# Performance work log

Measured on AMD Instinct MI355X. Metric: run time of the kernel, lower is better.

## Reference

```python
import jax, jax.numpy as jnp
import numpy as np

# Model dims (see init_kwargs / shape_source)
B = 2048      # batch
CIN = 256     # tabular input features (c_in)
NH = 512      # TabularEncoder hidden width
NENC_HID = 4  # nlayers=6 -> input layer + 4 hidden + output layer
NF = 112      # n_features = num_concepts (conv=False path)
K = 112       # num_concepts
NL = 50       # num_latent_concepts
MC = 100      # num_monte_carlo
NOUT = 200    # num_output


def setup_inputs() -> dict:
    key = jax.random.key(0)
    ks = jax.random.split(key, 8)
    x = jax.random.normal(ks[0], (B, CIN), dtype=jnp.float32)
    enc_Win = jax.random.normal(ks[1], (CIN, NH), dtype=jnp.float32) * (1.0 / np.sqrt(CIN))
    enc_bin = jnp.zeros((NH,), jnp.float32)
    enc_Wh = jax.random.normal(ks[2], (NENC_HID, NH, NH), dtype=jnp.float32) * (1.0 / np.sqrt(NH))
    enc_bh = jnp.zeros((NENC_HID, NH), jnp.float32)
    enc_Wout = jax.random.normal(ks[3], (NH, NF), dtype=jnp.float32) * (1.0 / np.sqrt(NH))
    enc_bout = jnp.zeros((NF,), jnp.float32)
    # Per-concept predictor i has first Linear of shape [NF+i, NL]; pad all to [NF+K, NL]
    # and statically slice rows [:NF+i] in the loop (unused padded rows never touched).
    pred_W1 = jax.random.normal(ks[4], (K, NF + K, NL), dtype=jnp.float32) * (1.0 / np.sqrt(NF))
    pred_b1 = jnp.zeros((K, NL), jnp.float32)
    pred_W2 = jax.random.normal(ks[5], (K, NL), dtype=jnp.float32) * (1.0 / np.sqrt(NL))
    pred_b2 = jnp.zeros((K,), jnp.float32)
    head_W = jax.random.normal(ks[6], (K, NOUT), dtype=jnp.float32) * (1.0 / np.sqrt(K))
    head_b = jnp.zeros((NOUT,), jnp.float32)
    return {
        "x": x,
        "enc_Win": enc_Win, "enc_bin": enc_bin,
        "enc_Wh": enc_Wh, "enc_bh": enc_bh,
        "enc_Wout": enc_Wout, "enc_bout": enc_bout,
        "pred_W1": pred_W1, "pred_b1": pred_b1,
        "pred_W2": pred_W2, "pred_b2": pred_b2,
        "head_W": head_W, "head_b": head_b,
        "epoch": 0,
    }


def reference(x, enc_Win, enc_bin, enc_Wh, enc_bh, enc_Wout, enc_bout,
              pred_W1, pred_b1, pred_W2, pred_b2, head_W, head_b, epoch):
    lrelu = jax.nn.leaky_relu  # negative_slope=0.01, matches nn.LeakyReLU default

    # ---- TabularEncoder (ni=CIN, nhidden=NH, nlayers=6, no=NF) ----
    h = lrelu(x @ enc_Win + enc_bin)
    for i in range(enc_Wh.shape[0]):
        h = lrelu(h @ enc_Wh[i] + enc_bh[i])
    inter = h @ enc_Wout + enc_bout                      # [B, NF]
    Bn = inter.shape[0]

    key = jax.random.key(42)
    c_hard = jnp.zeros((Bn, K, MC), inter.dtype)
    c_probs = []
    for i in range(K):
        W1 = pred_W1[i, :NF + i]                          # [NF+i, NL]
        base = inter @ W1[:NF] + pred_b1[i]               # [B, NL], shared across MC
        if i == 0:
            p1 = jax.nn.sigmoid(lrelu(base) @ pred_W2[i] + pred_b2[i])   # [B]
            p = jnp.broadcast_to(p1[:, None], (Bn, MC))   # expand(-1,-1,MC)
        else:
            # add contribution of the i previously sampled hard concepts, per MC sample
            hpre = base[:, None, :] + jnp.einsum('bim,ih->bmh', c_hard[:, :i], W1[NF:])  # [B,MC,NL]
            p = jax.nn.sigmoid(jnp.einsum('bmh,h->bm', lrelu(hpre), pred_W2[i]) + pred_b2[i])  # [B,MC]
        key, sk = jax.random.split(key)
        samp = jax.random.bernoulli(sk, p).astype(p.dtype)  # torch.bernoulli(concept)
        c_hard = c_hard.at[:, i, :].set(samp)
        c_probs.append(p)

    c_prob = jnp.stack(c_probs, axis=1)                   # [B, K, MC]

    # ---- Head: MC average of softmax probabilities (pred_dim > 1 branch) ----
    logits = jnp.einsum('bkm,ko->bmo', c_hard, head_W) + head_b   # [B, MC, NOUT]
    probs = jax.nn.softmax(logits, axis=-1).mean(axis=1)          # [B, NOUT]
    y_pred_logits = jnp.log(probs + 1e-6)
    return (c_prob, y_pred_logits, c_hard)
```

## Files before the change

### kernel.cpp

```cpp
#include <hip/hip_runtime.h>

typedef unsigned int u32;
typedef unsigned short u16;
typedef unsigned long long u64;

#define YOFF  22937600ull
#define CHOFF 23347200ull

#define OFF_HA    0ull
#define OFF_HB    4194304ull
#define OFF_INTER 8388608ull

__host__ __device__ inline u32 rotl32_(u32 x, int r) { return (x << r) | (x >> (32 - r)); }
__host__ __device__ inline void tf2x32(u32 k0, u32 k1, u32 c0, u32 c1, u32& o0, u32& o1) {
  u32 ks0 = k0, ks1 = k1, ks2 = k0 ^ k1 ^ 0x1BD11BDAu;
  u32 x0 = c0 + ks0, x1 = c1 + ks1;
  const int RA[4] = {13, 15, 26, 6}, RB[4] = {17, 29, 16, 24};
  for (int i = 0; i < 5; ++i) {
    const int* R = (i & 1) ? RB : RA;
    for (int j = 0; j < 4; ++j) { x0 += x1; x1 = rotl32_(x1, R[j]); x1 ^= x0; }
    switch (i) {
      case 0: x0 += ks1; x1 += ks2 + 1u; break;
      case 1: x0 += ks2; x1 += ks0 + 2u; break;
      case 2: x0 += ks0; x1 += ks1 + 3u; break;
      case 3: x0 += ks1; x1 += ks2 + 4u; break;
      case 4: x0 += ks2; x1 += ks0 + 5u; break;
    }
  }
  o0 = x0; o1 = x1;
}

struct SKeys { u32 v[224]; };

template <bool DO_LRELU>
__global__ __launch_bounds__(256) void gemm_bias(const float* __restrict__ A,
                                                 const float* __restrict__ Bm,
                                                 const float* __restrict__ bias,
                                                 float* __restrict__ C,
                                                 int M, int N, int K) {
  __shared__ float As[32][65];
  __shared__ float Bs[32][65];
  const int bm = blockIdx.y * 64, bn = blockIdx.x * 64;
  const int t = threadIdx.x;
  const int ty = t >> 4, tx = t & 15;
  float acc[4][4] = {};
  for (int k0 = 0; k0 < K; k0 += 32) {
#pragma unroll
    for (int l = 0; l < 2; ++l) {
      int e = l * 256 + t;
      int m = e >> 3, k4 = e & 7;
      float4 v = *(const float4*)(A + (size_t)(bm + m) * K + (k0 + k4 * 4));
      As[k4 * 4 + 0][m] = v.x; As[k4 * 4 + 1][m] = v.y;
      As[k4 * 4 + 2][m] = v.z; As[k4 * 4 + 3][m] = v.w;
    }
#pragma unroll
    for (int l = 0; l < 2; ++l) {
      int e = l * 256 + t;
      int k = e >> 4, n4 = e & 15;
      int gn = bn + n4 * 4;
      if (gn < N) {
        float4 v = *(const float4*)(Bm + (size_t)(k0 + k) * N + gn);
        Bs[k][n4 * 4 + 0] = v.x; Bs[k][n4 * 4 + 1] = v.y;
        Bs[k][n4 * 4 + 2] = v.z; Bs[k][n4 * 4 + 3] = v.w;
      } else {
        Bs[k][n4 * 4 + 0] = 0.f; Bs[k][n4 * 4 + 1] = 0.f;
        Bs[k][n4 * 4 + 2] = 0.f; Bs[k][n4 * 4 + 3] = 0.f;
      }
    }
    __syncthreads();
#pragma unroll
    for (int kk = 0; kk < 32; ++kk) {
      float a[4], b[4];
#pragma unroll
      for (int j = 0; j < 4; ++j) { a[j] = As[kk][ty * 4 + j]; b[j] = Bs[kk][tx * 4 + j]; }
#pragma unroll
      for (int i = 0; i < 4; ++i)
#pragma unroll
        for (int j = 0; j < 4; ++j) acc[i][j] = fmaf(a[i], b[j], acc[i][j]);
    }
    __syncthreads();
  }
#pragma unroll
  for (int i = 0; i < 4; ++i) {
#pragma unroll
    for (int j = 0; j < 4; ++j) {
      int m = bm + ty * 4 + i, n = bn + tx * 4 + j;
      if (n < N) {
        float s = acc[i][j] + bias[n];
        if (DO_LRELU) { if (s < 0.f) s = 0.01f * s; }
        C[(size_t)m * N + n] = s;
      }
    }
  }
}

__global__ __launch_bounds__(256) void base_kernel(const float* __restrict__ inter,
                                                   const float* __restrict__ W1,
                                                   const float* __restrict__ pb1,
                                                   float* __restrict__ out) {
  __shared__ float As[112][65];
  __shared__ float Ws[112][64];
  const int i = blockIdx.y;
  const int b0 = blockIdx.x * 64;
  const int t = threadIdx.x;
  const int ty = t >> 4, tx = t & 15;
#pragma unroll
  for (int l = 0; l < 7; ++l) {
    int e4 = l * 256 + t;
    int k4 = e4 % 28, bs = e4 / 28;
    float4 v = *(const float4*)(inter + (size_t)(b0 + bs) * 112 + k4 * 4);
    As[k4 * 4 + 0][bs] = v.x; As[k4 * 4 + 1][bs] = v.y;
    As[k4 * 4 + 2][bs] = v.z; As[k4 * 4 + 3][bs] = v.w;
  }
#pragma unroll
  for (int l = 0; l < 28; ++l) {
    int e = l * 256 + t;
    int r = e >> 6, c = e & 63;
    Ws[r][c] = (c < 50) ? W1[(size_t)i * 11200 + r * 50 + c] : 0.f;
  }
  __syncthreads();
  float acc[4][4] = {};
  for (int kk = 0; kk < 112; ++kk) {
    float a[4], b[4];
#pragma unroll
    for (int j = 0; j < 4; ++j) { a[j] = As[kk][ty * 4 + j]; b[j] = Ws[kk][tx * 4 + j]; }
#pragma unroll
    for (int ii = 0; ii < 4; ++ii)
#pragma unroll
      for (int j = 0; j < 4; ++j) acc[ii][j] = fmaf(a[ii], b[j], acc[ii][j]);
  }
#pragma unroll
  for (int ii = 0; ii < 4; ++ii) {
#pragma unroll
    for (int j = 0; j < 4; ++j) {
      int b = b0 + ty * 4 + ii, h = tx * 4 + j;
      if (h < 50) {
        out[CHOFF + (size_t)b * 11200 + (size_t)i * 100 + h] = acc[ii][j] + pb1[i * 50 + h];
      }
    }
  }
}

__global__ __launch_bounds__(512) void sample_kernel(const float* __restrict__ W1,
                                                     const float* __restrict__ W2,
                                                     const float* __restrict__ b2,
                                                     float* __restrict__ out, SKeys sks) {
  const int t = threadIdx.x;
  const int p = blockIdx.x * 500 + t;
  const bool active = (t < 500) && (p < 204800);
  const int b = p / 100;
  const int m = p - b * 100;
  const size_t rowbase = (size_t)b * 11200 + m;
  const float* __restrict__ baserow = out + CHOFF + (size_t)b * 11200;
  u64 lo = 0, hi = 0;

  if (active) {
    for (int i = 0; i < 112; ++i) {
      const float* __restrict__ Wi = W1 + (size_t)i * 11200 + 5600;
      float acc[50];
#pragma unroll
      for (int h = 0; h < 50; ++h) acc[h] = 0.f;
      for (int r = 0; r < i; ++r) {
        float c = (((r < 64) ? (lo >> r) : (hi >> (r - 64))) & 1ull) ? 1.f : 0.f;
        const float* __restrict__ wr = Wi + r * 50;
#pragma unroll
        for (int h = 0; h < 50; ++h) acc[h] = fmaf(c, wr[h], acc[h]);
      }
      const float* __restrict__ w2 = W2 + i * 50;
      const float* bs = baserow + (size_t)i * 100;
      float s = 0.f;
#pragma unroll
      for (int h = 0; h < 50; ++h) {
        float v = acc[h] + bs[h];
        if (v < 0.f) v = 0.01f * v;
        s = fmaf(v, w2[h], s);
      }
      float l = s + b2[i];
      float pr = 1.f / (1.f + expf(-l));
      u32 a0, a1;
      tf2x32(sks.v[2 * i], sks.v[2 * i + 1], 0u, (u32)p, a0, a1);
      u32 fb = ((a0 ^ a1) >> 9) | 0x3F800000u;
      float u; __builtin_memcpy(&u, &fb, 4); u -= 1.f;
      int smp = (u < pr) ? 1 : 0;
      out[rowbase + (size_t)i * 100] = pr;
      if (smp) { if (i < 64) lo |= 1ull << i; else hi |= 1ull << (i - 64); }
    }
    for (int i = 0; i < 112; ++i) {
      u64 bit = (i < 64) ? (lo >> i) : (hi >> (i - 64));
      out[CHOFF + rowbase + (size_t)i * 100] = (bit & 1ull) ? 1.0f : 0.0f;
    }
  }
}

__global__ __launch_bounds__(256) void head_kernel(const float* __restrict__ HW,
                                                   const float* __restrict__ hb,
                                                   float* __restrict__ out) {
  __shared__ unsigned char cS[100][116];
  __shared__ float lgS[50][201];
  const int b = blockIdx.x;
  const int t = threadIdx.x;
  for (int e = t; e < 11200; e += 256) {
    int k = e / 100, m = e - k * 100;
    cS[m][k] = (out[CHOFF + (size_t)b * 11200 + (size_t)k * 100 + m] != 0.f) ? 1 : 0;
  }
  __syncthreads();
  float pacc = 0.f;
  for (int mh = 0; mh < 2; ++mh) {
    for (int l = 0; l < 3; ++l) {
      int tile = l * 256 + t;
      if (tile < 625) {
        int o0 = (tile % 25) * 8;
        int m0 = (tile / 25) * 2;
        float acc[2][8] = {};
        for (int k = 0; k < 112; ++k) {
          float4 wa = *(const float4*)(HW + (size_t)k * 200 + o0);
          float4 wb = *(const float4*)(HW + (size_t)k * 200 + o0 + 4);
          float w[8] = {wa.x, wa.y, wa.z, wa.w, wb.x, wb.y, wb.z, wb.w};
          float c0 = (float)cS[mh * 50 + m0][k];
          float c1 = (float)cS[mh * 50 + m0 + 1][k];
#pragma unroll
          for (int jo = 0; jo < 8; ++jo) {
            acc[0][jo] = fmaf(c0, w[jo], acc[0][jo]);
            acc[1][jo] = fmaf(c1, w[jo], acc[1][jo]);
          }
        }
#pragma unroll
        for (int im = 0; im < 2; ++im)
#pragma unroll
          for (int jo = 0; jo < 8; ++jo) {
            int o = o0 + jo;
            lgS[m0 + im][o] = acc[im][jo] + hb[o];
          }
      }
    }
    __syncthreads();
    if (t < 50) {
      int m = t;
      float mx = -3.0e38f;
      for (int o = 0; o < 200; ++o) mx = fmaxf(mx, lgS[m][o]);
      float s = 0.f;
      for (int o = 0; o < 200; ++o) {
        float e = expf(lgS[m][o] - mx);
        lgS[m][o] = e; s += e;
      }
      float inv = 1.f / s;
      for (int o = 0; o < 200; ++o) lgS[m][o] = lgS[m][o] * inv;
    }
    __syncthreads();
    if (t < 200) { for (int m = 0; m < 50; ++m) pacc += lgS[m][t]; }
    __syncthreads();
  }
  if (t < 200) {
    out[YOFF + (size_t)b * 200 + t] = logf(pacc / 100.f + 1e-6f);
  }
}

extern "C" void kernel_launch(void* const* d_in, const int* in_sizes, int n_in,
                              void* d_out, int out_size, void* d_ws, size_t ws_size,
                              hipStream_t stream) {
  const float* x    = (const float*)d_in[0];
  const float* Win  = (const float*)d_in[1];
  const float* bin  = (const float*)d_in[2];
  const float* Wh   = (const float*)d_in[3];
  const float* bh   = (const float*)d_in[4];
  const float* Wout = (const float*)d_in[5];
  const float* bout = (const float*)d_in[6];
  const float* pW1  = (const float*)d_in[7];
  const float* pb1  = (const float*)d_in[8];
  const float* pW2  = (const float*)d_in[9];
  const float* pb2  = (const float*)d_in[10];
  const float* hW   = (const float*)d_in[11];
  const float* hb   = (const float*)d_in[12];
  float* out = (float*)d_out;
  char* ws = (char*)d_ws;

  float* hA     = (float*)(ws + OFF_HA);
  float* hB     = (float*)(ws + OFF_HB);
  float* interB = (float*)(ws + OFF_INTER);

  gemm_bias<true ><<<dim3(8, 32), 256, 0, stream>>>(x,  Win,             bin,          hA,     2048, 512, 256);
  gemm_bias<true ><<<dim3(8, 32), 256, 0, stream>>>(hA, Wh + 0 * 262144, bh + 0 * 512, hB,     2048, 512, 512);
  gemm_bias<true ><<<dim3(8, 32), 256, 0, stream>>>(hB, Wh + 1 * 262144, bh + 1 * 512, hA,     2048, 512, 512);
  gemm_bias<true ><<<dim3(8, 32), 256, 0, stream>>>(hA, Wh + 2 * 262144, bh + 2 * 512, hB,     2048, 512, 512);
  gemm_bias<true ><<<dim3(8, 32), 256, 0, stream>>>(hB, Wh + 3 * 262144, bh + 3 * 512, hA,     2048, 512, 512);
  gemm_bias<false><<<dim3(2, 32), 256, 0, stream>>>(hA, Wout,            bout,         interB, 2048, 112, 512);

  base_kernel<<<dim3(32, 112), 256, 0, stream>>>(interB, pW1, pb1, out);

  SKeys sks;
  {
    u32 k0 = 0u, k1 = 42u;
    for (int i = 0; i < 112; ++i) {
      u32 nk0, nk1, s0, s1;
      tf2x32(k0, k1, 0u, 0u, nk0, nk1);
      tf2x32(k0, k1, 0u, 1u, s0, s1);
      sks.v[2 * i] = s0; sks.v[2 * i + 1] = s1;
      k0 = nk0; k1 = nk1;
    }
  }
  sample_kernel<<<410, 512, 0, stream>>>(pW1, pW2, pb2, out, sks);

  head_kernel<<<2048, 256, 0, stream>>>(hW, hb, out);
}
```

Before: 3.718 ms.

## Split sequential sampling hidden dim across two warps and defer hard-concept expansion

Each (batch, MC) sample's 50-wide hidden accumulation in the sequential concept loop is now split across two wavefronts, 25 each, and partial activations are exchanged through shared memory every concept step. The goal is to cut per-thread register pressure and raise occupancy on the latency-bound serial loop, using 1600 blocks of 256 threads instead of 410 of 512. Sampled bits are packed into 32-bit words in scratch space within the c_hard region and expanded to floats by a separate kernel. The cost is two block barriers per concept iteration and an extra kernel launch.

Result: slower. 9.650 ms (+159.5%).

```diff
diff --git a/kernel.cpp b/kernel.cpp
--- a/kernel.cpp
+++ b/kernel.cpp
@@ -141,54 +141,121 @@
   }
 }
 
-__global__ __launch_bounds__(512) void sample_kernel(const float* __restrict__ W1,
-                                                     const float* __restrict__ W2,
-                                                     const float* __restrict__ b2,
-                                                     float* __restrict__ out, SKeys sks) {
-  const int t = threadIdx.x;
-  const int p = blockIdx.x * 500 + t;
-  const bool active = (t < 500) && (p < 204800);
+__global__ __launch_bounds__(256, 7) void sample_kernel2(const float* __restrict__ W1,
+                                                         const float* __restrict__ W2,
+                                                         const float* __restrict__ b2,
+                                                         float* __restrict__ out, SKeys sks) {
+  __shared__ float vbuf[128][26];
+  __shared__ u32 bitbuf[128];
+  const int t = threadIdx.x;
+  const int w = t >> 6;
+  const int lane = t & 63;
+  const int sub = w >> 1;
+  const int q = ((w & 1) << 6) | lane;
+  const int p = blockIdx.x * 128 + q;
   const int b = p / 100;
   const int m = p - b * 100;
-  const size_t rowbase = (size_t)b * 11200 + m;
   const float* __restrict__ baserow = out + CHOFF + (size_t)b * 11200;
   u64 lo = 0, hi = 0;
 
-  if (active) {
-    for (int i = 0; i < 112; ++i) {
-      const float* __restrict__ Wi = W1 + (size_t)i * 11200 + 5600;
-      float acc[50];
-#pragma unroll
-      for (int h = 0; h < 50; ++h) acc[h] = 0.f;
-      for (int r = 0; r < i; ++r) {
-        float c = (((r < 64) ? (lo >> r) : (hi >> (r - 64))) & 1ull) ? 1.f : 0.f;
+  for (int i = 0; i < 112; ++i) {
+    const float* __restrict__ Wi = W1 + (size_t)i * 11200 + 5600 + sub * 25;
+    float acc[25];
+#pragma unroll
+    for (int h = 0; h < 25; ++h) acc[h] = 0.f;
+    {
+      int r = 0;
+      int r1 = (i < 64) ? i : 64;
+      u64 cm = lo;
+      for (; r < r1; ++r) {
+        float c = (cm & 1ull) ? 1.f : 0.f;
+        cm >>= 1;
         const float* __restrict__ wr = Wi + r * 50;
 #pragma unroll
-        for (int h = 0; h < 50; ++h) acc[h] = fmaf(c, wr[h], acc[h]);
-      }
-      const float* __restrict__ w2 = W2 + i * 50;
-      const float* bs = baserow + (size_t)i * 100;
-      float s = 0.f;
-#pragma unroll
-      for (int h = 0; h < 50; ++h) {
-        float v = acc[h] + bs[h];
-        if (v < 0.f) v = 0.01f * v;
-        s = fmaf(v, w2[h], s);
-      }
-      float l = s + b2[i];
-      float pr = 1.f / (1.f + expf(-l));
+        for (int h = 0; h < 25; ++h) acc[h] = fmaf(c, wr[h], acc[h]);
+      }
+      cm = hi;
+      for (; r < i; ++r) {
+        float c = (cm & 1ull) ? 1.f : 0.f;
+        cm >>= 1;
+        const float* __restrict__ wr = Wi + r * 50;
+#pragma unroll
+        for (int h = 0; h < 25; ++h) acc[h] = fmaf(c, wr[h], acc[h]);
+      }
+    }
+    const float* bs = baserow + (size_t)i * 100 + sub * 25;
+    if (sub) {
+#pragma unroll
+      for (int h2 = 0; h2 < 12; ++h2) {
+        float v0 = acc[2 * h2] + bs[2 * h2];         if (v0 < 0.f) v0 = 0.01f * v0;
+        float v1 = acc[2 * h2 + 1] + bs[2 * h2 + 1]; if (v1 < 0.f) v1 = 0.01f * v1;
+        *(float2*)&vbuf[q][2 * h2] = make_float2(v0, v1);
+      }
+      {
+        float v24 = acc[24] + bs[24]; if (v24 < 0.f) v24 = 0.01f * v24;
+        vbuf[q][24] = v24;
+      }
       u32 a0, a1;
       tf2x32(sks.v[2 * i], sks.v[2 * i + 1], 0u, (u32)p, a0, a1);
       u32 fb = ((a0 ^ a1) >> 9) | 0x3F800000u;
       float u; __builtin_memcpy(&u, &fb, 4); u -= 1.f;
-      int smp = (u < pr) ? 1 : 0;
-      out[rowbase + (size_t)i * 100] = pr;
-      if (smp) { if (i < 64) lo |= 1ull << i; else hi |= 1ull << (i - 64); }
-    }
-    for (int i = 0; i < 112; ++i) {
-      u64 bit = (i < 64) ? (lo >> i) : (hi >> (i - 64));
-      out[CHOFF + rowbase + (size_t)i * 100] = (bit & 1ull) ? 1.0f : 0.0f;
-    }
+      vbuf[q][25] = u;
+    }
+    __syncthreads();
+    if (!sub) {
+      const float* __restrict__ w2 = W2 + i * 50;
+      float s = 0.f;
+#pragma unroll
+      for (int h = 0; h < 25; ++h) {
+        float v = acc[h] + bs[h];
+        if (v < 0.f) v = 0.01f * v;
+        s = fmaf(v, w2[h], s);
+      }
+#pragma unroll
+      for (int h2 = 0; h2 < 12; ++h2) {
+        float2 vv = *(const float2*)&vbuf[q][2 * h2];
+        s = fmaf(vv.x, w2[25 + 2 * h2], s);
+        s = fmaf(vv.y, w2[26 + 2 * h2], s);
+      }
+      s = fmaf(vbuf[q][24], w2[49], s);
+      float l = s + b2[i];
+      float pr = 1.f / (1.f + expf(-l));
+      float u = vbuf[q][25];
+      u32 smp = (u < pr) ? 1u : 0u;
+      out[(size_t)b * 11200 + (size_t)i * 100 + m] = pr;
+      bitbuf[q] = smp;
+    }
+    __syncthreads();
+    u32 bit = bitbuf[q];
+    if (bit) { if (i < 64) lo |= 1ull << i; else hi |= 1ull << (i - 64); }
+  }
+  if (!sub) {
+    u32* ob = (u32*)out;
+    size_t cb = CHOFF + (size_t)b * 11200 + (size_t)((m >= 50) ? 4 : 0) * 100 + 50 + (m % 50);
+    ob[cb + 0]   = (u32)lo;
+    ob[cb + 100] = (u32)(lo >> 32);
+    ob[cb + 200] = (u32)hi;
+    ob[cb + 300] = (u32)(hi >> 32);
+  }
+}
+
+__global__ __launch_bounds__(256) void expand_kernel(float* __restrict__ out) {
+  __shared__ u32 mW[100][4];
+  const int b = blockIdx.x;
+  const int t = threadIdx.x;
+  const u32* ob = (const u32*)out;
+  if (t < 100) {
+    size_t cb = CHOFF + (size_t)b * 11200 + (size_t)((t >= 50) ? 4 : 0) * 100 + 50 + (t % 50);
+    mW[t][0] = ob[cb + 0];
+    mW[t][1] = ob[cb + 100];
+    mW[t][2] = ob[cb + 200];
+    mW[t][3] = ob[cb + 300];
+  }
+  __syncthreads();
+  for (int e = t; e < 11200; e += 256) {
+    int i = e / 100, m = e - i * 100;
+    u32 word = mW[m][i >> 5];
+    out[CHOFF + (size_t)b * 11200 + e] = (float)((word >> (i & 31)) & 1u);
   }
 }
 
@@ -298,7 +365,8 @@
       k0 = nk0; k1 = nk1;
     }
   }
-  sample_kernel<<<410, 512, 0, stream>>>(pW1, pW2, pb2, out, sks);
+  sample_kernel2<<<1600, 256, 0, stream>>>(pW1, pW2, pb2, out, sks);
+  expand_kernel<<<2048, 256, 0, stream>>>(out);
 
   head_kernel<<<2048, 256, 0, stream>>>(hW, hb, out);
 }
```

## Double-buffer sample accumulators to overlap next-step matvec with current sampling

Applied to the files above, without the earlier changes.

Restructures the sequential concept-sampling kernel so that the contribution of all previous hard concepts to step i+1 is accumulated while step i is being finalized. Only the newest sampled bit is applied afterwards, which shortens the dependent chain per step. The bitmask is packed into scratch slots and expanded to floats by a new kernel, instead of 112 strided float stores per thread. The launch moves to 256-thread blocks with an occupancy hint, at the cost of two 50-float accumulator arrays of register pressure and an extra kernel launch.

Measured after the change: 8.867 ms. +138.5%, slower.

```diff
diff --git a/kernel.cpp b/kernel.cpp
--- a/kernel.cpp
+++ b/kernel.cpp
@@ -141,54 +141,116 @@
   }
 }
 
-__global__ __launch_bounds__(512) void sample_kernel(const float* __restrict__ W1,
-                                                     const float* __restrict__ W2,
-                                                     const float* __restrict__ b2,
-                                                     float* __restrict__ out, SKeys sks) {
-  const int t = threadIdx.x;
-  const int p = blockIdx.x * 500 + t;
-  const bool active = (t < 500) && (p < 204800);
+__global__ __launch_bounds__(256, 3) void sample_kernel3(const float* __restrict__ W1,
+                                                         const float* __restrict__ W2,
+                                                         const float* __restrict__ b2v,
+                                                         float* __restrict__ out, SKeys sks) {
+  const int t = threadIdx.x;
+  const int p = blockIdx.x * 256 + t;
   const int b = p / 100;
   const int m = p - b * 100;
-  const size_t rowbase = (size_t)b * 11200 + m;
   const float* __restrict__ baserow = out + CHOFF + (size_t)b * 11200;
   u64 lo = 0, hi = 0;
-
-  if (active) {
-    for (int i = 0; i < 112; ++i) {
-      const float* __restrict__ Wi = W1 + (size_t)i * 11200 + 5600;
-      float acc[50];
-#pragma unroll
-      for (int h = 0; h < 50; ++h) acc[h] = 0.f;
-      for (int r = 0; r < i; ++r) {
-        float c = (((r < 64) ? (lo >> r) : (hi >> (r - 64))) & 1ull) ? 1.f : 0.f;
-        const float* __restrict__ wr = Wi + r * 50;
-#pragma unroll
-        for (int h = 0; h < 50; ++h) acc[h] = fmaf(c, wr[h], acc[h]);
-      }
-      const float* __restrict__ w2 = W2 + i * 50;
-      const float* bs = baserow + (size_t)i * 100;
-      float s = 0.f;
-#pragma unroll
-      for (int h = 0; h < 50; ++h) {
-        float v = acc[h] + bs[h];
-        if (v < 0.f) v = 0.01f * v;
-        s = fmaf(v, w2[h], s);
-      }
-      float l = s + b2[i];
-      float pr = 1.f / (1.f + expf(-l));
-      u32 a0, a1;
-      tf2x32(sks.v[2 * i], sks.v[2 * i + 1], 0u, (u32)p, a0, a1);
-      u32 fb = ((a0 ^ a1) >> 9) | 0x3F800000u;
-      float u; __builtin_memcpy(&u, &fb, 4); u -= 1.f;
-      int smp = (u < pr) ? 1 : 0;
-      out[rowbase + (size_t)i * 100] = pr;
-      if (smp) { if (i < 64) lo |= 1ull << i; else hi |= 1ull << (i - 64); }
-    }
-    for (int i = 0; i < 112; ++i) {
-      u64 bit = (i < 64) ? (lo >> i) : (hi >> (i - 64));
-      out[CHOFF + rowbase + (size_t)i * 100] = (bit & 1ull) ? 1.0f : 0.0f;
-    }
+  float accA[50], accB[50];
+#pragma unroll
+  for (int h = 0; h < 50; ++h) accA[h] = 0.f;
+
+#define STEP(I, ACC_C, ACC_N)                                                               \
+  {                                                                                         \
+    const int i = (I);                                                                      \
+      \
+    if (i < 111) {                                                                          \
+      const float* __restrict__ Wn = W1 + (size_t)(i + 1) * 11200 + 5600;                   \
+      _Pragma("unroll")                                                                     \
+      for (int h = 0; h < 50; ++h) ACC_N[h] = 0.f;                                          \
+      _Pragma("unroll")                                                                     \
+      for (int half = 0; half < 2; ++half) {                                                \
+        const float* __restrict__ Wh = Wn + half * 25;                                      \
+        int r = 0;                                                                          \
+        int r1 = (i < 64) ? i : 64;                                                         \
+        u64 cm = lo;                                                                        \
+        for (; r < r1; ++r) {                                                               \
+          float c = (cm & 1ull) ? 1.f : 0.f;                                                \
+          cm >>= 1;                                                                         \
+          const float* __restrict__ wr = Wh + r * 50;       \
+          _Pragma("unroll")                                                                 \
+          for (int h = 0; h < 25; ++h)                                                      \
+            ACC_N[half * 25 + h] = fmaf(c, wr[h], ACC_N[half * 25 + h]);                    \
+        }                                                                                   \
+        cm = hi;                                                                            \
+        for (; r < i; ++r) {                                                                \
+          float c = (cm & 1ull) ? 1.f : 0.f;                                                \
+          cm >>= 1;                                                                         \
+          const float* __restrict__ wr = Wh + r * 50;                                       \
+          _Pragma("unroll")                                                                 \
+          for (int h = 0; h < 25; ++h)                                                      \
+            ACC_N[half * 25 + h] = fmaf(c, wr[h], ACC_N[half * 25 + h]);                    \
+        }                                                                                   \
+      }                                                                                     \
+    }                                                                                       \
+          \
+    const float* __restrict__ w2 = W2 + i * 50;                           \
+    const float* bs = baserow + (size_t)i * 100;           \
+    float s = 0.f;                                                                          \
+    _Pragma("unroll")                                                                       \
+    for (int h = 0; h < 50; ++h) {                                                          \
+      float v = ACC_C[h] + bs[h];                                                           \
+      if (v < 0.f) v = 0.01f * v;                                                           \
+      s = fmaf(v, w2[h], s);                                                                \
+    }                                                                                       \
+    float l = s + b2v[i];                                                                   \
+    float pr = 1.f / (1.f + expf(-l));                                                      \
+    u32 a0, a1;                                                                             \
+    tf2x32(sks.v[2 * i], sks.v[2 * i + 1], 0u, (u32)p, a0, a1);                             \
+    u32 fb = ((a0 ^ a1) >> 9) | 0x3F800000u;                                                \
+    float uu; __builtin_memcpy(&uu, &fb, 4); uu -= 1.f;                                     \
+    float cbit = (uu < pr) ? 1.f : 0.f;                                                     \
+    out[(size_t)b * 11200 + (size_t)i * 100 + m] = pr;             \
+    {                                                                                       \
+      u64 sbit = (uu < pr) ? 1ull : 0ull;                                                   \
+      if (i < 64) lo |= sbit << i; else hi |= sbit << (i - 64);                             \
+    }                                                                                       \
+         \
+    if (i < 111) {                                                                          \
+      const float* __restrict__ wr = W1 + (size_t)(i + 1) * 11200 + 5600 + (size_t)i * 50;  \
+      _Pragma("unroll")                                                                     \
+      for (int h = 0; h < 50; ++h) ACC_N[h] = fmaf(cbit, wr[h], ACC_N[h]);                  \
+    }                                                                                       \
+  }
+
+  for (int i0 = 0; i0 < 112; i0 += 2) {
+    STEP(i0, accA, accB)
+    STEP(i0 + 1, accB, accA)
+  }
+#undef STEP
+
+  {
+    u32* ob = (u32*)out;
+    size_t cb = CHOFF + (size_t)b * 11200 + (size_t)((m >= 50) ? 4 : 0) * 100 + 50 + (m % 50);
+    ob[cb + 0]   = (u32)lo;
+    ob[cb + 100] = (u32)(lo >> 32);
+    ob[cb + 200] = (u32)hi;
+    ob[cb + 300] = (u32)(hi >> 32);
+  }
+}
+
+__global__ __launch_bounds__(256) void expand_kernel(float* __restrict__ out) {
+  __shared__ u32 mW[100][4];
+  const int b = blockIdx.x;
+  const int t = threadIdx.x;
+  const u32* ob = (const u32*)out;
+  if (t < 100) {
+    size_t cb = CHOFF + (size_t)b * 11200 + (size_t)((t >= 50) ? 4 : 0) * 100 + 50 + (t % 50);
+    mW[t][0] = ob[cb + 0];
+    mW[t][1] = ob[cb + 100];
+    mW[t][2] = ob[cb + 200];
+    mW[t][3] = ob[cb + 300];
+  }
+  __syncthreads();
+  for (int e = t; e < 11200; e += 256) {
+    int i = e / 100, m = e - i * 100;
+    u32 word = mW[m][i >> 5];
+    out[CHOFF + (size_t)b * 11200 + e] = (float)((word >> (i & 31)) & 1u);
   }
 }
 
@@ -298,7 +360,8 @@
       k0 = nk0; k1 = nk1;
     }
   }
-  sample_kernel<<<410, 512, 0, stream>>>(pW1, pW2, pb2, out, sks);
+  sample_kernel3<<<800, 256, 0, stream>>>(pW1, pW2, pb2, out, sks);
+  expand_kernel<<<2048, 256, 0, stream>>>(out);
 
   head_kernel<<<2048, 256, 0, stream>>>(hW, hb, out);
 }
```

## Split sample kernel hidden dim across thread pairs with repacked padded W1

Applied to the files above, without the earlier changes.

The sequential Bernoulli sampling kernel now assigns two threads per (batch, MC) sample, each handling 25 of the 50 hidden units and combining partial results through a lane shuffle. W1's concept rows are repacked into a padded 56-wide layout so weights load as float4. The base values are stored in a matching padded column layout. Sampled bits go to a compact mask buffer, and a separate expand kernel writes the float hard-concept output. The aim is more parallelism and occupancy (1600 blocks, fewer registers per thread) with vectorised loads, at the cost of an extra repack pass, an extra expand kernel and shuffle traffic.

Measured after the change: 9.523 ms. +156.1%, slower.

```diff
diff --git a/kernel.cpp b/kernel.cpp
--- a/kernel.cpp
+++ b/kernel.cpp
@@ -94,6 +94,16 @@
   }
 }
 
+__global__ __launch_bounds__(256) void repack_w1(const float* __restrict__ W1, float* __restrict__ Wp) {
+  const int i = blockIdx.x;
+  for (int e = threadIdx.x; e < 112 * 56; e += 256) {
+    int r = e / 56, c = e - r * 56;
+    int sub = c / 28, h = c - sub * 28;
+    float v = (h < 25) ? W1[(size_t)i * 11200 + 5600 + r * 50 + sub * 25 + h] : 0.f;
+    Wp[(size_t)i * 6272 + e] = v;
+  }
+}
+
 __global__ __launch_bounds__(256) void base_kernel(const float* __restrict__ inter,
                                                    const float* __restrict__ W1,
                                                    const float* __restrict__ pb1,
@@ -135,60 +145,140 @@
     for (int j = 0; j < 4; ++j) {
       int b = b0 + ty * 4 + ii, h = tx * 4 + j;
       if (h < 50) {
-        out[CHOFF + (size_t)b * 11200 + (size_t)i * 100 + h] = acc[ii][j] + pb1[i * 50 + h];
-      }
-    }
-  }
-}
-
-__global__ __launch_bounds__(512) void sample_kernel(const float* __restrict__ W1,
-                                                     const float* __restrict__ W2,
-                                                     const float* __restrict__ b2,
-                                                     float* __restrict__ out, SKeys sks) {
-  const int t = threadIdx.x;
-  const int p = blockIdx.x * 500 + t;
-  const bool active = (t < 500) && (p < 204800);
+        int col = (h < 25) ? h : h + 3;
+        out[CHOFF + (size_t)b * 11200 + (size_t)i * 100 + col] = acc[ii][j] + pb1[i * 50 + h];
+      }
+    }
+  }
+}
+
+__global__ __launch_bounds__(256, 5) void sample_kernel4(const float* __restrict__ Wp,
+                                                         const float* __restrict__ W2,
+                                                         const float* __restrict__ b2v,
+                                                         float* __restrict__ out,
+                                                         u32* __restrict__ masks, SKeys sks) {
+  const int t = threadIdx.x;
+  const int sub = t & 1;
+  const int p = blockIdx.x * 128 + (t >> 1);
   const int b = p / 100;
   const int m = p - b * 100;
-  const size_t rowbase = (size_t)b * 11200 + m;
-  const float* __restrict__ baserow = out + CHOFF + (size_t)b * 11200;
+  const float* __restrict__ baseb = out + CHOFF + (size_t)b * 11200 + sub * 28;
+  const float* __restrict__ Wsub = Wp + sub * 28;
   u64 lo = 0, hi = 0;
-
-  if (active) {
-    for (int i = 0; i < 112; ++i) {
-      const float* __restrict__ Wi = W1 + (size_t)i * 11200 + 5600;
-      float acc[50];
-#pragma unroll
-      for (int h = 0; h < 50; ++h) acc[h] = 0.f;
-      for (int r = 0; r < i; ++r) {
-        float c = (((r < 64) ? (lo >> r) : (hi >> (r - 64))) & 1ull) ? 1.f : 0.f;
-        const float* __restrict__ wr = Wi + r * 50;
-#pragma unroll
-        for (int h = 0; h < 50; ++h) acc[h] = fmaf(c, wr[h], acc[h]);
-      }
-      const float* __restrict__ w2 = W2 + i * 50;
-      const float* bs = baserow + (size_t)i * 100;
-      float s = 0.f;
-#pragma unroll
-      for (int h = 0; h < 50; ++h) {
-        float v = acc[h] + bs[h];
-        if (v < 0.f) v = 0.01f * v;
-        s = fmaf(v, w2[h], s);
-      }
-      float l = s + b2[i];
-      float pr = 1.f / (1.f + expf(-l));
-      u32 a0, a1;
-      tf2x32(sks.v[2 * i], sks.v[2 * i + 1], 0u, (u32)p, a0, a1);
-      u32 fb = ((a0 ^ a1) >> 9) | 0x3F800000u;
-      float u; __builtin_memcpy(&u, &fb, 4); u -= 1.f;
-      int smp = (u < pr) ? 1 : 0;
-      out[rowbase + (size_t)i * 100] = pr;
-      if (smp) { if (i < 64) lo |= 1ull << i; else hi |= 1ull << (i - 64); }
-    }
-    for (int i = 0; i < 112; ++i) {
-      u64 bit = (i < 64) ? (lo >> i) : (hi >> (i - 64));
-      out[CHOFF + rowbase + (size_t)i * 100] = (bit & 1ull) ? 1.0f : 0.0f;
-    }
+  float acc[25], rcv[25];
+
+  for (int i = 0; i < 112; ++i) {
+#pragma unroll
+    for (int h = 0; h < 25; ++h) acc[h] = 0.f;
+    {
+      const float* __restrict__ Wi = Wsub + (size_t)i * 6272;
+      int r = 0;
+      int r1 = (i < 64) ? i : 64;
+      u64 cm = lo;
+      for (; r < r1; ++r) {
+        float c = (cm & 1ull) ? 1.f : 0.f;
+        cm >>= 1;
+        const float* __restrict__ wr = Wi + r * 56;
+        float4 q0 = ((const float4*)wr)[0];
+        float4 q1 = ((const float4*)wr)[1];
+        float4 q2 = ((const float4*)wr)[2];
+        float4 q3 = ((const float4*)wr)[3];
+        float4 q4 = ((const float4*)wr)[4];
+        float4 q5 = ((const float4*)wr)[5];
+        float w24 = wr[24];
+        acc[0] = fmaf(c, q0.x, acc[0]);  acc[1] = fmaf(c, q0.y, acc[1]);
+        acc[2] = fmaf(c, q0.z, acc[2]);  acc[3] = fmaf(c, q0.w, acc[3]);
+        acc[4] = fmaf(c, q1.x, acc[4]);  acc[5] = fmaf(c, q1.y, acc[5]);
+        acc[6] = fmaf(c, q1.z, acc[6]);  acc[7] = fmaf(c, q1.w, acc[7]);
+        acc[8] = fmaf(c, q2.x, acc[8]);  acc[9] = fmaf(c, q2.y, acc[9]);
+        acc[10] = fmaf(c, q2.z, acc[10]); acc[11] = fmaf(c, q2.w, acc[11]);
+        acc[12] = fmaf(c, q3.x, acc[12]); acc[13] = fmaf(c, q3.y, acc[13]);
+        acc[14] = fmaf(c, q3.z, acc[14]); acc[15] = fmaf(c, q3.w, acc[15]);
+        acc[16] = fmaf(c, q4.x, acc[16]); acc[17] = fmaf(c, q4.y, acc[17]);
+        acc[18] = fmaf(c, q4.z, acc[18]); acc[19] = fmaf(c, q4.w, acc[19]);
+        acc[20] = fmaf(c, q5.x, acc[20]); acc[21] = fmaf(c, q5.y, acc[21]);
+        acc[22] = fmaf(c, q5.z, acc[22]); acc[23] = fmaf(c, q5.w, acc[23]);
+        acc[24] = fmaf(c, w24, acc[24]);
+      }
+      cm = hi;
+      for (; r < i; ++r) {
+        float c = (cm & 1ull) ? 1.f : 0.f;
+        cm >>= 1;
+        const float* __restrict__ wr = Wi + r * 56;
+        float4 q0 = ((const float4*)wr)[0];
+        float4 q1 = ((const float4*)wr)[1];
+        float4 q2 = ((const float4*)wr)[2];
+        float4 q3 = ((const float4*)wr)[3];
+        float4 q4 = ((const float4*)wr)[4];
+        float4 q5 = ((const float4*)wr)[5];
+        float w24 = wr[24];
+        acc[0] = fmaf(c, q0.x, acc[0]);  acc[1] = fmaf(c, q0.y, acc[1]);
+        acc[2] = fmaf(c, q0.z, acc[2]);  acc[3] = fmaf(c, q0.w, acc[3]);
+        acc[4] = fmaf(c, q1.x, acc[4]);  acc[5] = fmaf(c, q1.y, acc[5]);
+        acc[6] = fmaf(c, q1.z, acc[6]);  acc[7] = fmaf(c, q1.w, acc[7]);
+        acc[8] = fmaf(c, q2.x, acc[8]);  acc[9] = fmaf(c, q2.y, acc[9]);
+        acc[10] = fmaf(c, q2.z, acc[10]); acc[11] = fmaf(c, q2.w, acc[11]);
+        acc[12] = fmaf(c, q3.x, acc[12]); acc[13] = fmaf(c, q3.y, acc[13]);
+        acc[14] = fmaf(c, q3.z, acc[14]); acc[15] = fmaf(c, q3.w, acc[15]);
+        acc[16] = fmaf(c, q4.x, acc[16]); acc[17] = fmaf(c, q4.y, acc[17]);
+        acc[18] = fmaf(c, q4.z, acc[18]); acc[19] = fmaf(c, q4.w, acc[19]);
+        acc[20] = fmaf(c, q5.x, acc[20]); acc[21] = fmaf(c, q5.y, acc[21]);
+        acc[22] = fmaf(c, q5.z, acc[22]); acc[23] = fmaf(c, q5.w, acc[23]);
+        acc[24] = fmaf(c, w24, acc[24]);
+      }
+    }
+    {
+      const float* __restrict__ bs = baseb + (size_t)i * 100;
+#pragma unroll
+      for (int j = 0; j < 6; ++j) {
+        float4 q = ((const float4*)bs)[j];
+        float x;
+        x = acc[4 * j + 0] + q.x; acc[4 * j + 0] = (x < 0.f) ? 0.01f * x : x;
+        x = acc[4 * j + 1] + q.y; acc[4 * j + 1] = (x < 0.f) ? 0.01f * x : x;
+        x = acc[4 * j + 2] + q.z; acc[4 * j + 2] = (x < 0.f) ? 0.01f * x : x;
+        x = acc[4 * j + 3] + q.w; acc[4 * j + 3] = (x < 0.f) ? 0.01f * x : x;
+      }
+      float x = acc[24] + bs[24]; acc[24] = (x < 0.f) ? 0.01f * x : x;
+    }
+#pragma unroll
+    for (int h = 0; h < 25; ++h) rcv[h] = __shfl_xor(acc[h], 1, 64);
+    const float* __restrict__ w2 = W2 + i * 50;
+    float s = 0.f;
+#pragma unroll
+    for (int h = 0; h < 25; ++h) { float val = sub ? rcv[h] : acc[h]; s = fmaf(val, w2[h], s); }
+#pragma unroll
+    for (int h = 0; h < 25; ++h) { float val = sub ? acc[h] : rcv[h]; s = fmaf(val, w2[25 + h], s); }
+    float l = s + b2v[i];
+    float pr = 1.f / (1.f + expf(-l));
+    u32 a0, a1;
+    tf2x32(sks.v[2 * i], sks.v[2 * i + 1], 0u, (u32)p, a0, a1);
+    u32 fb = ((a0 ^ a1) >> 9) | 0x3F800000u;
+    float uu; __builtin_memcpy(&uu, &fb, 4); uu -= 1.f;
+    u64 sbit = (uu < pr) ? 1ull : 0ull;
+    if (!sub) out[(size_t)b * 11200 + (size_t)i * 100 + m] = pr;
+    if (i < 64) lo |= sbit << i; else hi |= sbit << (i - 64);
+  }
+  if (!sub) {
+    u32* mp = masks + (size_t)p * 4;
+    mp[0] = (u32)lo; mp[1] = (u32)(lo >> 32);
+    mp[2] = (u32)hi; mp[3] = (u32)(hi >> 32);
+  }
+}
+
+__global__ __launch_bounds__(256) void expand_kernel(const u32* __restrict__ masks,
+                                                     float* __restrict__ out) {
+  __shared__ u32 mW[100][4];
+  const int b = blockIdx.x;
+  const int t = threadIdx.x;
+  if (t < 100) {
+    const u32* mp = masks + ((size_t)b * 100 + t) * 4;
+    mW[t][0] = mp[0]; mW[t][1] = mp[1]; mW[t][2] = mp[2]; mW[t][3] = mp[3];
+  }
+  __syncthreads();
+  for (int e = t; e < 11200; e += 256) {
+    int i = e / 100, m = e - i * 100;
+    u32 word = mW[m][i >> 5];
+    out[CHOFF + (size_t)b * 11200 + e] = (float)((word >> (i & 31)) & 1u);
   }
 }
 
@@ -277,6 +367,8 @@
   float* hA     = (float*)(ws + OFF_HA);
   float* hB     = (float*)(ws + OFF_HB);
   float* interB = (float*)(ws + OFF_INTER);
+  float* Wp     = (float*)(ws + OFF_HA);
+  u32*   masks  = (u32*)(ws + OFF_HB);
 
   gemm_bias<true ><<<dim3(8, 32), 256, 0, stream>>>(x,  Win,             bin,          hA,     2048, 512, 256);
   gemm_bias<true ><<<dim3(8, 32), 256, 0, stream>>>(hA, Wh + 0 * 262144, bh + 0 * 512, hB,     2048, 512, 512);
@@ -284,6 +376,8 @@
   gemm_bias<true ><<<dim3(8, 32), 256, 0, stream>>>(hA, Wh + 2 * 262144, bh + 2 * 512, hB,     2048, 512, 512);
   gemm_bias<true ><<<dim3(8, 32), 256, 0, stream>>>(hB, Wh + 3 * 262144, bh + 3 * 512, hA,     2048, 512, 512);
   gemm_bias<false><<<dim3(2, 32), 256, 0, stream>>>(hA, Wout,            bout,         interB, 2048, 112, 512);
+
+  repack_w1<<<112, 256, 0, stream>>>(pW1, Wp);
 
   base_kernel<<<dim3(32, 112), 256, 0, stream>>>(interB, pW1, pb1, out);
 
@@ -298,7 +392,8 @@
       k0 = nk0; k1 = nk1;
     }
   }
-  sample_kernel<<<410, 512, 0, stream>>>(pW1, pW2, pb2, out, sks);
+  sample_kernel4<<<1600, 256, 0, stream>>>(Wp, pW2, pb2, out, masks, sks);
+  expand_kernel<<<2048, 256, 0, stream>>>(masks, out);
 
   head_kernel<<<2048, 256, 0, stream>>>(hW, hb, out);
 }
```
